# Optimization experiments

Hardware: AMD Instinct MI355X
Metric: run time of the kernel (lower is better)

Reference implementation:

```python
import jax, jax.numpy as jnp
import numpy as np

H = 512      # cfg.hidden_size
I = 512      # input_size
T = 64       # cfg.recurrence
B = 1024     # num_trajectories

def setup_inputs() -> dict:
    key = jax.random.key(0)
    ks = jax.random.split(key, 7)
    s = 1.0 / np.sqrt(H)
    head_output = jax.random.normal(ks[0], (B * T, I), jnp.float32)
    rnn_states = jax.random.normal(ks[1], (B, 2 * H), jnp.float32)
    dones = jax.random.randint(ks[2], (B * T,), 0, 2).astype(jnp.float32)
    W_ih = jax.random.uniform(ks[3], (4 * H, I), jnp.float32, -s, s)
    W_hh = jax.random.uniform(ks[4], (4 * H, H), jnp.float32, -s, s)
    b_ih = jax.random.uniform(ks[5], (4 * H,), jnp.float32, -s, s)
    b_hh = jax.random.uniform(ks[6], (4 * H,), jnp.float32, -s, s)
    return {"head_output": head_output, "rnn_states": rnn_states, "dones": dones,
            "W_ih": W_ih, "W_hh": W_hh, "b_ih": b_ih, "b_hh": b_hh}

def reference(head_output, rnn_states, dones, W_ih, W_hh, b_ih, b_hh):
    # h, c: [B, H] each (num_layers == 1)
    h0, c0 = jnp.split(rnn_states, 2, axis=1)
    x_seq = head_output.reshape(B, T, I).transpose(1, 0, 2)  # [T, B, I]
    # is_new_episode = dones rolled by 1 along time, first step forced to 0
    d = dones.reshape(B, T)
    is_new = jnp.roll(d, 1, axis=1).at[:, 0].set(0.0)  # [B, T]
    masks = is_new.T  # [T, B]
    # precompute input projection for all steps (same math, hoisted out of the loop)
    x_proj = jnp.einsum('tbi,gi->tbg', x_seq, W_ih) + b_ih + b_hh  # [T, B, 4H]

    def step(carry, inp):
        h, c = carry
        xp, m = inp
        keep = (1.0 - m)[:, None]  # zero state at episode boundaries
        h = h * keep
        c = c * keep
        gates = xp + h @ W_hh.T  # [B, 4H], torch gate order i,f,g,o
        i_g, f_g, g_g, o_g = jnp.split(gates, 4, axis=1)
        i_g = jax.nn.sigmoid(i_g)
        f_g = jax.nn.sigmoid(f_g)
        g_g = jnp.tanh(g_g)
        o_g = jax.nn.sigmoid(o_g)
        c = f_g * c + i_g * g_g
        h = o_g * jnp.tanh(c)
        return (h, c), (h, c)

    (hT, cT), (hs, cs) = jax.lax.scan(step, (h0, c0), (x_proj, masks))
    # outputs at each step are h (output of single-layer LSTM)
    x = hs.transpose(1, 0, 2).reshape(B * T, H)  # [B*T, H]
    new_rnn_states = jnp.concatenate((hT, cT), axis=1)  # [B, 2H]
    h_stack = hs[:, None, :, :]  # [T, 1, B, H] (num_layers dim)
    c_stack = cs[:, None, :, :]
    return x, new_rnn_states, (h_stack, c_stack)
```

## Files before the change

### kernel.cpp

```cpp
#include <hip/hip_runtime.h>
#include <stdint.h>


#define WC_OFF   0u
#define HF_OFF   4194304u
#define CF_OFF   5242880u
#define BIAS_OFF 7340032u
#define F_WIH   0u
#define F_WHH   2097152u
#define F_HF0   4194304u
#define F_HF1   5242880u
#define F_BIAS  6291456u
#define F_CTR   6299648u
#define F_XBF   7340032u
#define F_XPROJ 74448896u
#define F_NEED  342884352u
#define OUT_RNN  33554432u
#define OUT_HS   34603008u
#define OUT_CS   68157440u

typedef __attribute__((ext_vector_type(4))) float f32x4;
typedef __attribute__((ext_vector_type(8))) short s16x8;
typedef __attribute__((ext_vector_type(4))) unsigned int u32x4;
typedef __attribute__((ext_vector_type(4))) unsigned short u16x4;

__device__ __forceinline__ unsigned short f2bf(float f) {
  union { float f; unsigned int u; } v; v.f = f;
  return (unsigned short)((v.u + 0x7FFFu + ((v.u >> 16) & 1u)) >> 16);
}
__device__ __forceinline__ float bf2f(unsigned short s) {
  union { unsigned int u; float f; } v; v.u = ((unsigned int)s) << 16;
  return v.f;
}
__device__ __forceinline__ unsigned int pack2(float a, float b) {
  return (unsigned int)f2bf(a) | ((unsigned int)f2bf(b) << 16);
}
__device__ __forceinline__ float sigm(float x) { return 1.0f / (1.0f + __expf(-x)); }

__device__ __forceinline__ void gl_lds16(const void* g, void* lds) {
  __builtin_amdgcn_global_load_lds(
      (const __attribute__((address_space(1))) unsigned int*)g,
      (__attribute__((address_space(3))) unsigned int*)lds, 16, 0, 0);
}

__device__ __forceinline__ void lds_barrier() {
  asm volatile("s_waitcnt lgkmcnt(0)" ::: "memory");
  __builtin_amdgcn_sched_barrier(0);
  __builtin_amdgcn_s_barrier();
}



__global__ void __launch_bounds__(256) prep_fast(
    const float* __restrict__ xg, const float* __restrict__ rnn,
    const float* __restrict__ Wih, const float* __restrict__ Whh,
    const float* __restrict__ bih, const float* __restrict__ bhh,
    unsigned char* __restrict__ ws) {
  unsigned int tid = blockIdx.x * 256u + threadIdx.x;
  unsigned short* wih_f = (unsigned short*)(ws + F_WIH);
  unsigned short* whh_f = (unsigned short*)(ws + F_WHH);
  float* bias = (float*)(ws + F_BIAS);
  unsigned short* xbf = (unsigned short*)(ws + F_XBF);
  if (tid < 131072u) {
    unsigned int frag = tid >> 6, l = tid & 63u;
    unsigned int cb = frag >> 4, ks = frag & 15u;
    unsigned int g  = cb * 16u + (l & 15u);
    unsigned int k0 = ks * 32u + ((l >> 4) << 3);
    const float* src = Wih + (size_t)g * 512u + k0;
    u32x4 p;
    p.x = pack2(src[0], src[1]); p.y = pack2(src[2], src[3]);
    p.z = pack2(src[4], src[5]); p.w = pack2(src[6], src[7]);
    *(u32x4*)(wih_f + (size_t)frag * 512u + l * 8u) = p;
  } else if (tid < 262144u) {
    unsigned int t2 = tid - 131072u;
    unsigned int frag = t2 >> 6, l = t2 & 63u;
    unsigned int cb = frag >> 4, ks = frag & 15u;
    unsigned int g  = cb * 16u + (l & 15u);
    unsigned int k0 = ks * 32u + ((l >> 4) << 3);
    const float* src = Whh + (size_t)g * 512u + k0;
    u32x4 p;
    p.x = pack2(src[0], src[1]); p.y = pack2(src[2], src[3]);
    p.z = pack2(src[4], src[5]); p.w = pack2(src[6], src[7]);
    *(u32x4*)(whh_f + (size_t)frag * 512u + l * 8u) = p;
  } else if (tid < 327680u) {
    unsigned int t2 = tid - 262144u;
    unsigned int frag = t2 >> 6, l = t2 & 63u;
    unsigned int mb = frag >> 4, ks = frag & 15u;
    unsigned int b  = mb * 16u + (l & 15u);
    unsigned int c0 = ks * 32u + ((l >> 4) << 3);
    const float* src = rnn + (size_t)b * 1024u + c0;
    union { u32x4 v; unsigned long long q[2]; } u;
    u.v.x = pack2(src[0], src[1]); u.v.y = pack2(src[2], src[3]);
    u.v.z = pack2(src[4], src[5]); u.v.w = pack2(src[6], src[7]);
    unsigned long long* hq = (unsigned long long*)(ws + F_HF0);
    hq[(size_t)frag * 128u + l] = u.q[0];
    hq[(size_t)frag * 128u + 64u + l] = u.q[1];
  } else if (tid < 329728u) {
    unsigned int g = tid - 327680u;
    bias[g] = bih[g] + bhh[g];
  } else if (tid < 329744u) {
    __hip_atomic_store((unsigned int*)(ws + F_CTR) + (tid - 329728u) * 32u, 0u,
                       __ATOMIC_RELAXED, __HIP_MEMORY_SCOPE_AGENT);
  } else if (tid >= 331776u && tid < 4526080u) {
    unsigned int t2 = tid - 331776u;
    unsigned int frag = t2 >> 6, l = t2 & 63u;
    unsigned int ks = frag & 15u, mb = (frag >> 4) & 63u, t = frag >> 10;
    unsigned int b  = mb * 16u + (l & 15u);
    unsigned int k0 = ks * 32u + ((l >> 4) << 3);
    const float* src = xg + ((size_t)(b * 64u + t)) * 512u + k0;
    u32x4 p;
    p.x = pack2(src[0], src[1]); p.y = pack2(src[2], src[3]);
    p.z = pack2(src[4], src[5]); p.w = pack2(src[6], src[7]);
    *(u32x4*)(xbf + (size_t)frag * 512u + l * 8u) = p;
  }
}

__global__ void __launch_bounds__(256) gemm_xproj(unsigned char* __restrict__ ws) {
  const unsigned short* xbf = (const unsigned short*)(ws + F_XBF);
  const unsigned short* wih = (const unsigned short*)(ws + F_WIH);
  const float* bias = (const float*)(ws + F_BIAS);
  unsigned short* xproj = (unsigned short*)(ws + F_XPROJ);

  __shared__ __align__(16) unsigned char smem[65536];
  const int tid = threadIdx.x;
  const int w = tid >> 6, l = tid & 63;
  const int mh = w & 1, nh = w >> 1;
  const int bid = blockIdx.x;
  const int t = bid >> 7, mtile = (bid >> 4) & 7, ntile = bid & 15;

  f32x4 acc[4][4];
  {
    f32x4 z = {0.f, 0.f, 0.f, 0.f};
    #pragma unroll
    for (int i = 0; i < 4; ++i)
      #pragma unroll
      for (int j = 0; j < 4; ++j) acc[i][j] = z;
  }

  auto stage = [&](int kc, int buf) {
    unsigned char* ab = smem + buf * 16384;
    unsigned char* bb = smem + 32768 + buf * 16384;
    #pragma unroll
    for (int j = 0; j < 4; ++j) {
      int idx = w * 4 + j;
      int mb_l = idx >> 1, ksl = idx & 1;
      size_t frag = (size_t)(t * 64 + mtile * 8 + mb_l) * 16u + kc * 2 + ksl;
      gl_lds16(xbf + (frag * 64u + l) * 8u, ab + idx * 1024);
    }
    #pragma unroll
    for (int j = 0; j < 4; ++j) {
      int idx = w * 4 + j;
      int cb_l = idx >> 1, ksl = idx & 1;
      size_t frag = (size_t)(ntile * 8 + cb_l) * 16u + kc * 2 + ksl;
      gl_lds16(wih + (frag * 64u + l) * 8u, bb + idx * 1024);
    }
  };

  stage(0, 0);
  __syncthreads();
  for (int kc = 0; kc < 8; ++kc) {
    int cur = kc & 1;
    if (kc < 7) stage(kc + 1, cur ^ 1);
    unsigned char* ab = smem + cur * 16384;
    unsigned char* bb = smem + 32768 + cur * 16384;
    s16x8 afr[4][2], bfr[4][2];
    #pragma unroll
    for (int m = 0; m < 4; ++m)
      #pragma unroll
      for (int ksl = 0; ksl < 2; ++ksl)
        afr[m][ksl] = *(const s16x8*)(ab + ((mh * 4 + m) * 2 + ksl) * 1024 + l * 16);
    #pragma unroll
    for (int n = 0; n < 4; ++n)
      #pragma unroll
      for (int ksl = 0; ksl < 2; ++ksl)
        bfr[n][ksl] = *(const s16x8*)(bb + ((nh * 4 + n) * 2 + ksl) * 1024 + l * 16);
    #pragma unroll
    for (int m = 0; m < 4; ++m)
      #pragma unroll
      for (int n = 0; n < 4; ++n)
        #pragma unroll
        for (int ksl = 0; ksl < 2; ++ksl)
          acc[m][n] = __builtin_amdgcn_mfma_f32_16x16x32_bf16(
              afr[m][ksl], bfr[n][ksl], acc[m][n], 0, 0, 0);
    __syncthreads();
  }

  #pragma unroll
  for (int m = 0; m < 4; ++m) {
    int mb_abs = mtile * 8 + mh * 4 + m;
    #pragma unroll
    for (int n = 0; n < 4; ++n) {
      int n_abs = ntile * 8 + nh * 4 + n;
      float bc = bias[n_abs * 16 + (l & 15)];
      u16x4 p;
      #pragma unroll
      for (int r = 0; r < 4; ++r) p[r] = f2bf(acc[m][n][r] + bc);
      *(u16x4*)(xproj + ((size_t)(t * 64 + mb_abs) * 128u + n_abs) * 256u + l * 4u) = p;
    }
  }
}

#define P_HL  131072
#define P_CL  141312
#define P_DN  151552
__global__ void __launch_bounds__(512, 2) persist_lock(
    const float* __restrict__ rnn, const float* __restrict__ dones,
    unsigned char* __restrict__ ws, float* __restrict__ out) {
  const unsigned short* whh = (const unsigned short*)(ws + F_WHH);
  const unsigned short* xproj = (const unsigned short*)(ws + F_XPROJ);
  unsigned int* ctrs = (unsigned int*)(ws + F_CTR);
  unsigned long long* hq0 = (unsigned long long*)(ws + F_HF0);
  unsigned long long* hq1 = (unsigned long long*)(ws + F_HF1);

  __shared__ __align__(16) unsigned char smem[160768];
  float* Hl = (float*)(smem + P_HL);
  float* Cl = (float*)(smem + P_CL);
  unsigned short* dn16 = (unsigned short*)(smem + P_DN);

  const int tid = threadIdx.x;
  const int w = tid >> 6, l = tid & 63;
  const int mbw = w >> 1, cbl = w & 1;
  const int mt = (int)blockIdx.x & 15, ht = (int)blockIdx.x >> 4;

  #pragma unroll
  for (int j = 0; j < 16; ++j) {
    int idx = w * 16 + j;
    int gcb = idx >> 4, ks = idx & 15;
    int cb = (gcb >> 1) * 32 + ht * 2 + (gcb & 1);
    gl_lds16(whh + ((size_t)(cb * 16 + ks) * 64u + l) * 8u, smem + idx * 1024);
  }
  {
    const float* dsrc = dones + (size_t)mt * 4096u + tid * 8;
    f32x4 d0 = *(const f32x4*)dsrc, d1 = *(const f32x4*)(dsrc + 4);
    int row = tid >> 3, t0 = (tid & 7) * 8;
    u32x4 p;
    p.x = pack2(d0.x, d0.y); p.y = pack2(d0.z, d0.w);
    p.z = pack2(d1.x, d1.y); p.w = pack2(d1.z, d1.w);
    *(u32x4*)(dn16 + row * 72 + t0) = p;
  }
  f32x4 cold;
  #pragma unroll
  for (int r = 0; r < 4; ++r) {
    int b = mt * 64 + mbw * 16 + ((l >> 4) << 2) + r;
    cold[r] = rnn[(size_t)b * 1024u + 512u + ht * 32 + cbl * 16 + (l & 15)];
  }
  __syncthreads();

  #pragma unroll 1
  for (int t = 0; t < 64; ++t) {
    const unsigned long long* hsrc = (t & 1) ? hq1 : hq0;
    unsigned long long* hdst = (t & 1) ? hq0 : hq1;

    s16x8 areg[16];
    #pragma unroll
    for (int ks = 0; ks < 16; ++ks) {
      size_t f = (size_t)((mt * 4 + mbw) * 16 + ks) * 128u;
      union { unsigned long long q[2]; s16x8 v; } u;
      u.q[0] = __hip_atomic_load(hsrc + f + l,
                                 __ATOMIC_RELAXED, __HIP_MEMORY_SCOPE_AGENT);
      u.q[1] = __hip_atomic_load(hsrc + f + 64u + l,
                                 __ATOMIC_RELAXED, __HIP_MEMORY_SCOPE_AGENT);
      areg[ks] = u.v;
    }
    u16x4 xq[4];
    #pragma unroll
    for (int g = 0; g < 4; ++g) {
      int n_abs = g * 32 + ht * 2 + cbl;
      xq[g] = __builtin_nontemporal_load((const u16x4*)(xproj +
          ((size_t)(t * 64 + mt * 4 + mbw) * 128u + n_abs) * 256u + l * 4u));
    }

    f32x4 acc[4];
    {
      f32x4 z = {0.f, 0.f, 0.f, 0.f};
      #pragma unroll
      for (int g = 0; g < 4; ++g) acc[g] = z;
    }
    #pragma unroll
    for (int ks = 0; ks < 16; ++ks) {
      s16x8 bfr[4];
      #pragma unroll
      for (int g = 0; g < 4; ++g)
        bfr[g] = *(const s16x8*)(smem + ((g * 2 + cbl) * 16 + ks) * 1024 + l * 16);
      #pragma unroll
      for (int g = 0; g < 4; ++g)
        acc[g] = __builtin_amdgcn_mfma_f32_16x16x32_bf16(areg[ks], bfr[g], acc[g], 0, 0, 0);
    }
    #pragma unroll
    for (int g = 0; g < 4; ++g)
      #pragma unroll
      for (int r = 0; r < 4; ++r) acc[g][r] += bf2f(xq[g][r]);

    #pragma unroll
    for (int r = 0; r < 4; ++r) {
      float gi = sigm(acc[0][r]);
      float gf = sigm(acc[1][r]);
      float gg = tanhf(acc[2][r]);
      float go = sigm(acc[3][r]);
      int lrow = mbw * 16 + ((l >> 4) << 2) + r;
      float cc = gf * cold[r] + gi * gg;
      float h = go * tanhf(cc);
      float keep = 1.0f - bf2f(dn16[lrow * 72 + t]);
      cold[r] = cc * keep;
      Hl[lrow * 40 + cbl * 16 + (l & 15)] = h;
      Cl[lrow * 40 + cbl * 16 + (l & 15)] = cc;
    }
    __syncthreads();

    if (t < 63) {
      if (tid < 256) {
        const int mbl = tid >> 6, lp = tid & 63;
        const int row = mbl * 16 + (lp & 15);
        const float keep = 1.0f - bf2f(dn16[row * 72 + t]);
        const float* hr = Hl + (size_t)row * 40u + ((lp >> 4) << 3);
        union { u32x4 v; unsigned long long q[2]; } u;
        u.v.x = pack2(hr[0] * keep, hr[1] * keep);
        u.v.y = pack2(hr[2] * keep, hr[3] * keep);
        u.v.z = pack2(hr[4] * keep, hr[5] * keep);
        u.v.w = pack2(hr[6] * keep, hr[7] * keep);
        size_t f = (size_t)((mt * 4 + mbl) * 16 + ht) * 128u;
        __hip_atomic_store(hdst + f + lp, u.q[0],
                           __ATOMIC_RELAXED, __HIP_MEMORY_SCOPE_AGENT);
        __hip_atomic_store(hdst + f + 64u + lp, u.q[1],
                           __ATOMIC_RELAXED, __HIP_MEMORY_SCOPE_AGENT);
      }
      __syncthreads();

      if (tid == 0) {
        unsigned int* ctr = ctrs + mt * 32;
        __hip_atomic_fetch_add(ctr, 1u, __ATOMIC_RELEASE, __HIP_MEMORY_SCOPE_AGENT);
        unsigned int target = 16u * (unsigned int)(t + 1);
        while (__hip_atomic_load(ctr, __ATOMIC_ACQUIRE, __HIP_MEMORY_SCOPE_AGENT) < target)
          __builtin_amdgcn_s_sleep(1);
      }
      {
        int row = tid >> 3, chn = tid & 7;
        int b = mt * 64 + row;
        f32x4 hv = *(const f32x4*)(Hl + row * 40 + chn * 4);
        f32x4 cv = *(const f32x4*)(Cl + row * 40 + chn * 4);
        int colg = ht * 32 + chn * 4;
        __builtin_nontemporal_store(hv, (f32x4*)(out + ((size_t)(b * 64 + t)) * 512u + colg));
        __builtin_nontemporal_store(hv, (f32x4*)(out + OUT_HS + ((size_t)(t * 1024 + b)) * 512u + colg));
        __builtin_nontemporal_store(cv, (f32x4*)(out + OUT_CS + ((size_t)(t * 1024 + b)) * 512u + colg));
      }
      lds_barrier();
    } else {
      int row = tid >> 3, chn = tid & 7;
      int b = mt * 64 + row;
      f32x4 hv = *(const f32x4*)(Hl + row * 40 + chn * 4);
      f32x4 cv = *(const f32x4*)(Cl + row * 40 + chn * 4);
      int colg = ht * 32 + chn * 4;
      __builtin_nontemporal_store(hv, (f32x4*)(out + ((size_t)(b * 64 + t)) * 512u + colg));
      __builtin_nontemporal_store(hv, (f32x4*)(out + OUT_HS + ((size_t)(t * 1024 + b)) * 512u + colg));
      __builtin_nontemporal_store(cv, (f32x4*)(out + OUT_CS + ((size_t)(t * 1024 + b)) * 512u + colg));
      __builtin_nontemporal_store(hv, (f32x4*)(out + OUT_RNN + (size_t)b * 1024u + colg));
      __builtin_nontemporal_store(cv, (f32x4*)(out + OUT_RNN + (size_t)b * 1024u + 512u + colg));
    }
  }
}


__global__ void __launch_bounds__(256) prep_kernel(
    const float* __restrict__ rnn, const float* __restrict__ Wih,
    const float* __restrict__ Whh, const float* __restrict__ bih,
    const float* __restrict__ bhh, unsigned char* __restrict__ ws) {
  unsigned int tid = blockIdx.x * 256u + threadIdx.x;
  unsigned short* wcf = (unsigned short*)(ws + WC_OFF);
  unsigned short* hf  = (unsigned short*)(ws + HF_OFF);
  float* cf   = (float*)(ws + CF_OFF);
  float* bias = (float*)(ws + BIAS_OFF);
  if (tid < 262144u) {
    unsigned int frag = tid >> 6, l = tid & 63u;
    unsigned int cb = frag >> 5, ks = frag & 31u;
    unsigned int g  = cb * 16u + (l & 15u);
    unsigned int k0 = ks * 32u + ((l >> 4) << 3);
    const float* src = (k0 < 512u) ? (Wih + g * 512u + k0) : (Whh + g * 512u + (k0 - 512u));
    u32x4 p;
    p.x = pack2(src[0], src[1]); p.y = pack2(src[2], src[3]);
    p.z = pack2(src[4], src[5]); p.w = pack2(src[6], src[7]);
    *(u32x4*)(wcf + (size_t)frag * 512u + l * 8u) = p;
  } else if (tid < 327680u) {
    unsigned int t2 = tid - 262144u;
    unsigned int frag = t2 >> 6, l = t2 & 63u;
    unsigned int mb = frag >> 4, ks = frag & 15u;
    unsigned int b  = mb * 16u + (l & 15u);
    unsigned int c0 = ks * 32u + ((l >> 4) << 3);
    const float* src = rnn + (size_t)b * 1024u + c0;
    u32x4 p;
    p.x = pack2(src[0], src[1]); p.y = pack2(src[2], src[3]);
    p.z = pack2(src[4], src[5]); p.w = pack2(src[6], src[7]);
    *(u32x4*)(hf + (size_t)frag * 512u + l * 8u) = p;
  } else if (tid < 458752u) {
    unsigned int t2 = tid - 327680u;
    unsigned int frag = t2 >> 6, l = t2 & 63u;
    unsigned int mb = frag >> 5, cfi = frag & 31u;
    unsigned int hcol = cfi * 16u + (l & 15u);
    f32x4 p;
    #pragma unroll
    for (int r = 0; r < 4; ++r) {
      unsigned int b = mb * 16u + ((l >> 4) << 2) + r;
      p[r] = rnn[(size_t)b * 1024u + 512u + hcol];
    }
    *(f32x4*)(cf + (size_t)frag * 256u + l * 4u) = p;
  } else if (tid < 460800u) {
    unsigned int g = tid - 458752u;
    bias[g] = bih[g] + bhh[g];
  }
}

__global__ void __launch_bounds__(256) step_kernel(
    const float* __restrict__ xg, const float* __restrict__ dones,
    unsigned char* __restrict__ ws, float* __restrict__ out, int t) {
  const unsigned short* wcf = (const unsigned short*)(ws + WC_OFF);
  unsigned short* hf = (unsigned short*)(ws + HF_OFF);
  float* cf = (float*)(ws + CF_OFF);
  const float* bias = (const float*)(ws + BIAS_OFF);

  __shared__ __align__(16) unsigned char smem[49152];
  const int tid = threadIdx.x;
  const int w = tid >> 6, l = tid & 63;
  const int mh = w & 1, ch = w >> 1;
  const int mt = (int)blockIdx.x >> 4, ht = (int)blockIdx.x & 15;

  f32x4 acc[2][4];
  {
    f32x4 z = {0.f, 0.f, 0.f, 0.f};
    #pragma unroll
    for (int i = 0; i < 2; ++i)
      #pragma unroll
      for (int j = 0; j < 4; ++j) acc[i][j] = z;
  }

  f32x4 xv[2][2];

  auto stage_load = [&](int kc, int buf) {
    unsigned char* bb = smem + 16384 + buf * 16384;
    #pragma unroll
    for (int j = 0; j < 4; ++j) {
      int idx = w * 4 + j;
      int g = idx >> 2, cbl = (idx >> 1) & 1, ksl = idx & 1;
      int cb = g * 32 + ht * 2 + cbl;
      int ks = kc * 2 + ksl;
      const unsigned short* src = wcf + ((size_t)(cb * 32 + ks) * 64u + l) * 8u;
      gl_lds16(src, bb + idx * 1024);
    }
    unsigned char* ab = smem + buf * 8192;
    if (kc >= 8) {
      #pragma unroll
      for (int j = 0; j < 2; ++j) {
        int idx = w * 2 + j;
        int ksh = (kc - 8) * 2 + j;
        int mb_abs = mt * 4 + w;
        const unsigned short* src = hf + ((size_t)(mb_abs * 16 + ksh) * 64u + l) * 8u;
        gl_lds16(src, ab + idx * 1024);
      }
    } else {
      #pragma unroll
      for (int j = 0; j < 2; ++j) {
        int ks = kc * 2 + j;
        int b = mt * 64 + w * 16 + (l & 15);
        int k0 = ks * 32 + ((l >> 4) << 3);
        const float* src = xg + ((size_t)(b * 64 + t)) * 512u + k0;
        xv[j][0] = *(const f32x4*)src;
        xv[j][1] = *(const f32x4*)(src + 4);
      }
    }
  };
  auto stage_write = [&](int kc, int buf) {
    if (kc < 8) {
      unsigned char* ab = smem + buf * 8192;
      #pragma unroll
      for (int j = 0; j < 2; ++j) {
        int idx = w * 2 + j;
        u32x4 p;
        p.x = pack2(xv[j][0].x, xv[j][0].y); p.y = pack2(xv[j][0].z, xv[j][0].w);
        p.z = pack2(xv[j][1].x, xv[j][1].y); p.w = pack2(xv[j][1].z, xv[j][1].w);
        *(u32x4*)(ab + idx * 1024 + l * 16) = p;
      }
    }
  };

  stage_load(0, 0);
  stage_write(0, 0);
  __syncthreads();

  for (int kc = 0; kc < 16; ++kc) {
    int cur = kc & 1;
    if (kc < 15) stage_load(kc + 1, cur ^ 1);
    unsigned char* ab = smem + cur * 8192;
    unsigned char* bb = smem + 16384 + cur * 16384;
    s16x8 afr[2][2], bfr[4][2];
    #pragma unroll
    for (int mb2 = 0; mb2 < 2; ++mb2)
      #pragma unroll
      for (int ksl = 0; ksl < 2; ++ksl)
        afr[mb2][ksl] = *(const s16x8*)(ab + ((mh * 2 + mb2) * 2 + ksl) * 1024 + l * 16);
    #pragma unroll
    for (int g = 0; g < 4; ++g)
      #pragma unroll
      for (int ksl = 0; ksl < 2; ++ksl)
        bfr[g][ksl] = *(const s16x8*)(bb + (g * 4 + ch * 2 + ksl) * 1024 + l * 16);
    #pragma unroll
    for (int mb2 = 0; mb2 < 2; ++mb2)
      #pragma unroll
      for (int g = 0; g < 4; ++g)
        #pragma unroll
        for (int ksl = 0; ksl < 2; ++ksl)
          acc[mb2][g] = __builtin_amdgcn_mfma_f32_16x16x32_bf16(
              afr[mb2][ksl], bfr[g][ksl], acc[mb2][g], 0, 0, 0);
    if (kc < 15) stage_write(kc + 1, cur ^ 1);
    __syncthreads();
  }

  const int hcol = ht * 32 + ch * 16 + (l & 15);
  const float bi = bias[hcol], bf2 = bias[512 + hcol];
  const float bg = bias[1024 + hcol], bo = bias[1536 + hcol];
  float* Hl = (float*)smem;
  float* Cl = (float*)(smem + 9216);
  const int cfi = ht * 2 + ch;
  const int colL = ch * 16 + (l & 15);
  #pragma unroll
  for (int mb2 = 0; mb2 < 2; ++mb2) {
    const int mb_abs = mt * 4 + mh * 2 + mb2;
    const int fid = mb_abs * 32 + cfi;
    f32x4 cold = *(const f32x4*)(cf + (size_t)fid * 256u + l * 4u);
    f32x4 cmask;
    #pragma unroll
    for (int r = 0; r < 4; ++r) {
      float gi = sigm(acc[mb2][0][r] + bi);
      float gf = sigm(acc[mb2][1][r] + bf2);
      float gg = tanhf(acc[mb2][2][r] + bg);
      float go = sigm(acc[mb2][3][r] + bo);
      float c = gf * cold[r] + gi * gg;
      float h = go * tanhf(c);
      int brow = mb_abs * 16 + ((l >> 4) << 2) + r;
      float keep = 1.0f - dones[brow * 64 + t];
      cmask[r] = c * keep;
      int rowL = mh * 32 + mb2 * 16 + ((l >> 4) << 2) + r;
      Hl[rowL * 36 + colL] = h;
      Cl[rowL * 36 + colL] = c;
    }
    *(f32x4*)(cf + (size_t)fid * 256u + l * 4u) = cmask;
  }
  __syncthreads();

  {
    const int mb2f = tid >> 6, lp = tid & 63;
    const int mb_abs = mt * 4 + mb2f;
    const int rowL = mb2f * 16 + (lp & 15);
    const int c0 = (lp >> 4) << 3;
    const int brow = mt * 64 + rowL;
    const float keep = 1.0f - dones[brow * 64 + t];
    const float* hr = Hl + rowL * 36 + c0;
    u32x4 p;
    p.x = pack2(hr[0] * keep, hr[1] * keep);
    p.y = pack2(hr[2] * keep, hr[3] * keep);
    p.z = pack2(hr[4] * keep, hr[5] * keep);
    p.w = pack2(hr[6] * keep, hr[7] * keep);
    *(u32x4*)(hf + ((size_t)(mb_abs * 16 + ht) * 64u + lp) * 8u) = p;
  }
  {
    const int row = tid & 63, cg2 = tid >> 6;
    const int b = mt * 64 + row;
    const int c0 = cg2 * 8;
    const float* hr = Hl + row * 36 + c0;
    const float* cr = Cl + row * 36 + c0;
    f32x4 h0 = *(const f32x4*)hr,  h1 = *(const f32x4*)(hr + 4);
    f32x4 cc0 = *(const f32x4*)cr, cc1 = *(const f32x4*)(cr + 4);
    const int colg = ht * 32 + c0;
    size_t xoff = ((size_t)(b * 64 + t)) * 512u + colg;
    *(f32x4*)(out + xoff) = h0; *(f32x4*)(out + xoff + 4) = h1;
    size_t hoff = OUT_HS + ((size_t)(t * 1024 + b)) * 512u + colg;
    *(f32x4*)(out + hoff) = h0; *(f32x4*)(out + hoff + 4) = h1;
    size_t coff = OUT_CS + ((size_t)(t * 1024 + b)) * 512u + colg;
    *(f32x4*)(out + coff) = cc0; *(f32x4*)(out + coff + 4) = cc1;
    if (t == 63) {
      size_t roff = OUT_RNN + (size_t)b * 1024u + colg;
      *(f32x4*)(out + roff) = h0;        *(f32x4*)(out + roff + 4) = h1;
      *(f32x4*)(out + roff + 512) = cc0; *(f32x4*)(out + roff + 516) = cc1;
    }
  }
}

extern "C" void kernel_launch(void* const* d_in, const int* in_sizes, int n_in,
                              void* d_out, int out_size, void* d_ws, size_t ws_size,
                              hipStream_t stream) {
  const float* xg  = (const float*)d_in[0];
  const float* rnn = (const float*)d_in[1];
  const float* dn  = (const float*)d_in[2];
  const float* Wih = (const float*)d_in[3];
  const float* Whh = (const float*)d_in[4];
  const float* bih = (const float*)d_in[5];
  const float* bhh = (const float*)d_in[6];
  float* out = (float*)d_out;
  unsigned char* ws = (unsigned char*)d_ws;
  (void)in_sizes; (void)n_in; (void)out_size;

  if (ws_size >= (size_t)F_NEED) {
    prep_fast<<<17680, 256, 0, stream>>>(xg, rnn, Wih, Whh, bih, bhh, ws);
    gemm_xproj<<<8192, 256, 0, stream>>>(ws);
    persist_lock<<<256, 512, 0, stream>>>(rnn, dn, ws, out);
  } else {
    prep_kernel<<<1800, 256, 0, stream>>>(rnn, Wih, Whh, bih, bhh, ws);
    for (int t = 0; t < 64; ++t)
      step_kernel<<<256, 256, 0, stream>>>(xg, dn, ws, out, t);
  }
}
```

Before: 1.232 ms.

## Spin per wave, prefetch next-step h and xproj, use fast gate activations

In the persistent recurrent LSTM kernel, the wait on the cross-block step counter moves from thread 0 (followed by a block barrier) to lane 0 of each wave. Each wave then issues the next step's h-fragment and x-projection loads right after its own wait, before the trailing LDS barrier. This aims to shorten the serial per-step critical path between blocks. Sigmoid and tanh are rewritten with the hardware reciprocal and exp, which is cheaper but less accurate than tanhf. The LDS row pitch for the H/C staging buffers drops from 40 to 36 floats, shrinking shared memory and changing the bank mapping.

```diff
diff --git a/kernel.cpp b/kernel.cpp
--- a/kernel.cpp
+++ b/kernel.cpp
@@ -36,6 +36,11 @@
   return (unsigned int)f2bf(a) | ((unsigned int)f2bf(b) << 16);
 }
 __device__ __forceinline__ float sigm(float x) { return 1.0f / (1.0f + __expf(-x)); }
+__device__ __forceinline__ float frcp(float x) { return __builtin_amdgcn_rcpf(x); }
+__device__ __forceinline__ float sigm_f(float x) { return frcp(1.0f + __expf(-x)); }
+__device__ __forceinline__ float tanh_f(float x) {
+  return 1.0f - 2.0f * frcp(1.0f + __expf(2.0f * x));
+}
 
 __device__ __forceinline__ void gl_lds16(const void* g, void* lds) {
   __builtin_amdgcn_global_load_lds(
@@ -201,8 +206,8 @@
 }
 
 #define P_HL  131072
-#define P_CL  141312
-#define P_DN  151552
+#define P_CL  140288
+#define P_DN  149504
 __global__ void __launch_bounds__(512, 2) persist_lock(
     const float* __restrict__ rnn, const float* __restrict__ dones,
     unsigned char* __restrict__ ws, float* __restrict__ out) {
@@ -212,7 +217,7 @@
   unsigned long long* hq0 = (unsigned long long*)(ws + F_HF0);
   unsigned long long* hq1 = (unsigned long long*)(ws + F_HF1);
 
-  __shared__ __align__(16) unsigned char smem[160768];
+  __shared__ __align__(16) unsigned char smem[158720];
   float* Hl = (float*)(smem + P_HL);
   float* Cl = (float*)(smem + P_CL);
   unsigned short* dn16 = (unsigned short*)(smem + P_DN);
@@ -221,6 +226,7 @@
   const int w = tid >> 6, l = tid & 63;
   const int mbw = w >> 1, cbl = w & 1;
   const int mt = (int)blockIdx.x & 15, ht = (int)blockIdx.x >> 4;
+  unsigned int* ctr = ctrs + mt * 32;
 
   #pragma unroll
   for (int j = 0; j < 16; ++j) {
@@ -246,30 +252,25 @@
   }
   __syncthreads();
 
+  s16x8 areg[16];
+  #pragma unroll
+  for (int ks = 0; ks < 16; ++ks) {
+    size_t f = (size_t)((mt * 4 + mbw) * 16 + ks) * 128u;
+    union { unsigned long long q[2]; s16x8 v; } u;
+    u.q[0] = __hip_atomic_load(hq0 + f + l, __ATOMIC_RELAXED, __HIP_MEMORY_SCOPE_AGENT);
+    u.q[1] = __hip_atomic_load(hq0 + f + 64u + l, __ATOMIC_RELAXED, __HIP_MEMORY_SCOPE_AGENT);
+    areg[ks] = u.v;
+  }
+  u16x4 xq[4];
+  #pragma unroll
+  for (int g = 0; g < 4; ++g) {
+    int n_abs = g * 32 + ht * 2 + cbl;
+    xq[g] = __builtin_nontemporal_load((const u16x4*)(xproj +
+        ((size_t)(0 * 64 + mt * 4 + mbw) * 128u + n_abs) * 256u + l * 4u));
+  }
+
   #pragma unroll 1
   for (int t = 0; t < 64; ++t) {
-    const unsigned long long* hsrc = (t & 1) ? hq1 : hq0;
-    unsigned long long* hdst = (t & 1) ? hq0 : hq1;
-
-    s16x8 areg[16];
-    #pragma unroll
-    for (int ks = 0; ks < 16; ++ks) {
-      size_t f = (size_t)((mt * 4 + mbw) * 16 + ks) * 128u;
-      union { unsigned long long q[2]; s16x8 v; } u;
-      u.q[0] = __hip_atomic_load(hsrc + f + l,
-                                 __ATOMIC_RELAXED, __HIP_MEMORY_SCOPE_AGENT);
-      u.q[1] = __hip_atomic_load(hsrc + f + 64u + l,
-                                 __ATOMIC_RELAXED, __HIP_MEMORY_SCOPE_AGENT);
-      areg[ks] = u.v;
-    }
-    u16x4 xq[4];
-    #pragma unroll
-    for (int g = 0; g < 4; ++g) {
-      int n_abs = g * 32 + ht * 2 + cbl;
-      xq[g] = __builtin_nontemporal_load((const u16x4*)(xproj +
-          ((size_t)(t * 64 + mt * 4 + mbw) * 128u + n_abs) * 256u + l * 4u));
-    }
-
     f32x4 acc[4];
     {
       f32x4 z = {0.f, 0.f, 0.f, 0.f};
@@ -293,26 +294,27 @@
 
     #pragma unroll
     for (int r = 0; r < 4; ++r) {
-      float gi = sigm(acc[0][r]);
-      float gf = sigm(acc[1][r]);
-      float gg = tanhf(acc[2][r]);
-      float go = sigm(acc[3][r]);
+      float gi = sigm_f(acc[0][r]);
+      float gf = sigm_f(acc[1][r]);
+      float gg = tanh_f(acc[2][r]);
+      float go = sigm_f(acc[3][r]);
       int lrow = mbw * 16 + ((l >> 4) << 2) + r;
       float cc = gf * cold[r] + gi * gg;
-      float h = go * tanhf(cc);
+      float h = go * tanh_f(cc);
       float keep = 1.0f - bf2f(dn16[lrow * 72 + t]);
       cold[r] = cc * keep;
-      Hl[lrow * 40 + cbl * 16 + (l & 15)] = h;
-      Cl[lrow * 40 + cbl * 16 + (l & 15)] = cc;
+      Hl[lrow * 36 + cbl * 16 + (l & 15)] = h;
+      Cl[lrow * 36 + cbl * 16 + (l & 15)] = cc;
     }
     __syncthreads();
 
     if (t < 63) {
+      unsigned long long* hdst = (t & 1) ? hq0 : hq1;
       if (tid < 256) {
         const int mbl = tid >> 6, lp = tid & 63;
         const int row = mbl * 16 + (lp & 15);
         const float keep = 1.0f - bf2f(dn16[row * 72 + t]);
-        const float* hr = Hl + (size_t)row * 40u + ((lp >> 4) << 3);
+        const float* hr = Hl + (size_t)row * 36u + ((lp >> 4) << 3);
         union { u32x4 v; unsigned long long q[2]; } u;
         u.v.x = pack2(hr[0] * keep, hr[1] * keep);
         u.v.y = pack2(hr[2] * keep, hr[3] * keep);
@@ -326,29 +328,48 @@
       }
       __syncthreads();
 
-      if (tid == 0) {
-        unsigned int* ctr = ctrs + mt * 32;
+      if (tid == 0)
         __hip_atomic_fetch_add(ctr, 1u, __ATOMIC_RELEASE, __HIP_MEMORY_SCOPE_AGENT);
-        unsigned int target = 16u * (unsigned int)(t + 1);
-        while (__hip_atomic_load(ctr, __ATOMIC_ACQUIRE, __HIP_MEMORY_SCOPE_AGENT) < target)
-          __builtin_amdgcn_s_sleep(1);
-      }
       {
         int row = tid >> 3, chn = tid & 7;
         int b = mt * 64 + row;
-        f32x4 hv = *(const f32x4*)(Hl + row * 40 + chn * 4);
-        f32x4 cv = *(const f32x4*)(Cl + row * 40 + chn * 4);
+        f32x4 hv = *(const f32x4*)(Hl + row * 36 + chn * 4);
+        f32x4 cv = *(const f32x4*)(Cl + row * 36 + chn * 4);
         int colg = ht * 32 + chn * 4;
         __builtin_nontemporal_store(hv, (f32x4*)(out + ((size_t)(b * 64 + t)) * 512u + colg));
         __builtin_nontemporal_store(hv, (f32x4*)(out + OUT_HS + ((size_t)(t * 1024 + b)) * 512u + colg));
         __builtin_nontemporal_store(cv, (f32x4*)(out + OUT_CS + ((size_t)(t * 1024 + b)) * 512u + colg));
       }
+      {
+        unsigned int target = 16u * (unsigned int)(t + 1);
+        if ((tid & 63) == 0) {
+          while (__hip_atomic_load(ctr, __ATOMIC_ACQUIRE, __HIP_MEMORY_SCOPE_AGENT) < target)
+            __builtin_amdgcn_s_sleep(1);
+        }
+      }
+      {
+        const unsigned long long* hnxt = ((t + 1) & 1) ? hq1 : hq0;
+        #pragma unroll
+        for (int ks = 0; ks < 16; ++ks) {
+          size_t f = (size_t)((mt * 4 + mbw) * 16 + ks) * 128u;
+          union { unsigned long long q[2]; s16x8 v; } u;
+          u.q[0] = __hip_atomic_load(hnxt + f + l, __ATOMIC_RELAXED, __HIP_MEMORY_SCOPE_AGENT);
+          u.q[1] = __hip_atomic_load(hnxt + f + 64u + l, __ATOMIC_RELAXED, __HIP_MEMORY_SCOPE_AGENT);
+          areg[ks] = u.v;
+        }
+        #pragma unroll
+        for (int g = 0; g < 4; ++g) {
+          int n_abs = g * 32 + ht * 2 + cbl;
+          xq[g] = __builtin_nontemporal_load((const u16x4*)(xproj +
+              ((size_t)((t + 1) * 64 + mt * 4 + mbw) * 128u + n_abs) * 256u + l * 4u));
+        }
+      }
       lds_barrier();
     } else {
       int row = tid >> 3, chn = tid & 7;
       int b = mt * 64 + row;
-      f32x4 hv = *(const f32x4*)(Hl + row * 40 + chn * 4);
-      f32x4 cv = *(const f32x4*)(Cl + row * 40 + chn * 4);
+      f32x4 hv = *(const f32x4*)(Hl + row * 36 + chn * 4);
+      f32x4 cv = *(const f32x4*)(Cl + row * 36 + chn * 4);
       int colg = ht * 32 + chn * 4;
       __builtin_nontemporal_store(hv, (f32x4*)(out + ((size_t)(b * 64 + t)) * 512u + colg));
       __builtin_nontemporal_store(hv, (f32x4*)(out + OUT_HS + ((size_t)(t * 1024 + b)) * 512u + colg));
```

New measurement: 2.908 ms. 2.36x slower.
